# Kernel optimization log

Measured on AMD Instinct MI355X. Metric: run time of the kernel, lower is better.

The kernel has to match this reference:

```python
import jax, jax.numpy as jnp
import numpy as np

N = 100000      # nodes
E = 1600000     # edges (before self-loops)
IN_C = 128
HID = 256
L = 4
EPS = 1e-5


def setup_inputs() -> dict:
    key = jax.random.key(0)
    ks = jax.random.split(key, 12)
    s = 0.05
    x = jax.random.normal(ks[0], (N, IN_C), dtype=jnp.float32)
    edge_index = jax.random.randint(ks[1], (2, E), 0, N, dtype=jnp.int64)
    enc_w = jax.random.normal(ks[2], (IN_C, HID), dtype=jnp.float32) * s
    enc_b = jnp.zeros((HID,), jnp.float32)
    conv_w = jax.random.normal(ks[3], (L, HID, HID), dtype=jnp.float32) * s
    conv_b = jnp.zeros((L, HID), jnp.float32)
    ln_g = jnp.ones((L, HID), jnp.float32)
    ln_b = jnp.zeros((L, HID), jnp.float32)
    lin1_w = jax.random.normal(ks[4], (HID, HID // 2), dtype=jnp.float32) * s
    lin1_b = jnp.zeros((HID // 2,), jnp.float32)
    lin2_w = jax.random.normal(ks[5], (HID // 2, 1), dtype=jnp.float32) * s
    lin2_b = jnp.zeros((1,), jnp.float32)
    return dict(x=x, edge_index=edge_index, enc_w=enc_w, enc_b=enc_b,
                conv_w=conv_w, conv_b=conv_b, ln_g=ln_g, ln_b=ln_b,
                lin1_w=lin1_w, lin1_b=lin1_b, lin2_w=lin2_w, lin2_b=lin2_b)


def _layer_norm(h, g, b):
    mu = jnp.mean(h, axis=-1, keepdims=True)
    var = jnp.mean(jnp.square(h - mu), axis=-1, keepdims=True)
    return (h - mu) * jax.lax.rsqrt(var + EPS) * g + b


def reference(x, edge_index, enc_w, enc_b, conv_w, conv_b, ln_g, ln_b,
              lin1_w, lin1_b, lin2_w, lin2_b):
    loops = jnp.arange(N, dtype=edge_index.dtype)
    row = jnp.concatenate([edge_index[0], loops])   # source
    col = jnp.concatenate([edge_index[1], loops])   # target
    # GCN symmetric norm with self-loop weight 1 (improved=False)
    deg = jax.ops.segment_sum(jnp.ones(row.shape[0], jnp.float32), col,
                              num_segments=N)
    dis = jnp.where(deg > 0, jax.lax.rsqrt(deg), 0.0)  # deg^-1/2, [N]

    h = x @ enc_w + enc_b
    for i in range(L):
        hw = h @ conv_w[i]
        # norm_e = dis[row]*dis[col]: scale at source, aggregate, scale at target
        agg = jax.ops.segment_sum((hw * dis[:, None])[row], col,
                                  num_segments=N)
        h = agg * dis[:, None] + conv_b[i]
        h = jax.nn.relu(_layer_norm(h, ln_g[i], ln_b[i]))
        # dropout p=0.1 is identity in eval mode
    h = jax.nn.relu(h @ lin1_w + lin1_b)
    return h @ lin2_w + lin2_b  # [N, 1]
```

## Files before the change

kernel.cpp:

```cpp
#include <hip/hip_runtime.h>

#define N_NODES 100000
#define N_EDGES 1600000
#define IN_C    128
#define HID     256
#define NLAYER  4

#define NBUCK 391
#define BCAP  8192
#define EPB   4096
#define CAPL  6144

typedef __attribute__((ext_vector_type(8))) __bf16 bf16x8;
typedef __attribute__((ext_vector_type(4))) float  floatx4;

__device__ inline unsigned short f2b(float f) {
    unsigned u = __builtin_bit_cast(unsigned, f);
    return (unsigned short)((u + 0x7fffu + ((u >> 16) & 1u)) >> 16);
}
__device__ inline void acc8(float* a, uint4 v) {
    unsigned wds[4] = {v.x, v.y, v.z, v.w};
    #pragma unroll
    for (int k = 0; k < 4; ++k) {
        a[2*k]   += __builtin_bit_cast(float, wds[k] << 16);
        a[2*k+1] += __builtin_bit_cast(float, wds[k] & 0xffff0000u);
    }
}
__device__ inline void gl16(const void* g, void* l) {
    __builtin_amdgcn_global_load_lds(
        (const __attribute__((address_space(1))) unsigned int*)g,
        (__attribute__((address_space(3))) unsigned int*)l, 16, 0, 0);
}

__global__ __launch_bounds__(256) void kb_scatter(
        const int* __restrict__ row, const int* __restrict__ col,
        int* __restrict__ gfill, uint2* __restrict__ pairs, int e) {
    __shared__ uint2 ep[EPB];
    __shared__ int hist[NBUCK];
    __shared__ int lbase[NBUCK];
    const int tid  = threadIdx.x;
    const int base = blockIdx.x * EPB;
    for (int b = tid; b < NBUCK; b += 256) hist[b] = 0;
    __syncthreads();
    #pragma unroll
    for (int k = 0; k < EPB / 256; ++k) {
        int i = base + k * 256 + tid;
        uint2 pr = make_uint2(0xffffffffu, 0u);
        if (i < e) {
            pr.x = (unsigned)col[i];
            pr.y = (unsigned)row[i];
            atomicAdd(&hist[pr.x >> 8], 1);
        }
        ep[k * 256 + tid] = pr;
    }
    __syncthreads();
    for (int b = tid; b < NBUCK; b += 256) {
        int h = hist[b];
        lbase[b] = h ? atomicAdd(&gfill[b], h) : 0;
    }
    __syncthreads();
    for (int b = tid; b < NBUCK; b += 256) hist[b] = 0;
    __syncthreads();
    #pragma unroll
    for (int k = 0; k < EPB / 256; ++k) {
        uint2 pr = ep[k * 256 + tid];
        if (pr.x != 0xffffffffu) {
            int bk = pr.x >> 8;
            int p  = lbase[bk] + atomicAdd(&hist[bk], 1);
            if (p < BCAP) pairs[(size_t)bk * BCAP + p] = pr;
        }
    }
}

__global__ void kb_scan(const int* __restrict__ gfill, int* __restrict__ boff,
                        int* __restrict__ offs) {
    __shared__ int wsum[8];
    const int t = threadIdx.x, lane = t & 63, w = t >> 6;
    int v = (t < NBUCK) ? gfill[t] : 0;
    int inc = v;
    #pragma unroll
    for (int o = 1; o < 64; o <<= 1) { int u = __shfl_up(inc, o); if (lane >= o) inc += u; }
    if (lane == 63) wsum[w] = inc;
    __syncthreads();
    if (t == 0) { int r = 0; for (int i = 0; i < 8; ++i) { int x = wsum[i]; wsum[i] = r; r += x; } }
    __syncthreads();
    int excl = wsum[w] + inc - v;
    if (t <= NBUCK) boff[t] = excl;
    if (t == 0) offs[N_NODES] = N_EDGES;
}

__global__ __launch_bounds__(256) void kb_build(
        const uint2* __restrict__ pairs, const int* __restrict__ gfill,
        const int* __restrict__ boff,
        int* __restrict__ offs, float* __restrict__ dis,
        int* __restrict__ srcl, int n) {
    __shared__ int lcnt[256];
    __shared__ int lstart[256];
    __shared__ int wsum[4];
    __shared__ int sl[CAPL];
    const int b = blockIdx.x;
    const int tid = threadIdx.x, lane = tid & 63, w = tid >> 6;
    int cnt = gfill[b]; if (cnt > CAPL) cnt = CAPL;
    const int base = boff[b];
    const uint2* bp = pairs + (size_t)b * BCAP;
    lcnt[tid] = 0;
    __syncthreads();
    for (int i = tid; i < cnt; i += 256)
        atomicAdd(&lcnt[bp[i].x & 255], 1);
    __syncthreads();
    int v = lcnt[tid];
    int inc = v;
    #pragma unroll
    for (int o = 1; o < 64; o <<= 1) { int u = __shfl_up(inc, o); if (lane >= o) inc += u; }
    if (lane == 63) wsum[w] = inc;
    __syncthreads();
    if (tid == 0) { int r = 0; for (int i = 0; i < 4; ++i) { int x = wsum[i]; wsum[i] = r; r += x; } }
    __syncthreads();
    int excl = wsum[w] + inc - v;
    lstart[tid] = excl;
    int node = (b << 8) + tid;
    if (node < n) {
        dis[node]  = rsqrtf((float)(v + 1));
        offs[node] = base + excl;
    }
    __syncthreads();
    lcnt[tid] = 0;
    __syncthreads();
    for (int i = tid; i < cnt; i += 256) {
        uint2 pr = bp[i];
        int c = pr.x & 255;
        int q = lstart[c] + atomicAdd(&lcnt[c], 1);
        sl[q] = (int)pr.y;
    }
    __syncthreads();
    for (int i = tid; i < cnt; i += 256)
        srcl[base + i] = sl[i];
}

__global__ void k_wtz(const float* __restrict__ enc_w, const float* __restrict__ conv_w,
                      const float* __restrict__ w1,
                      unsigned short* __restrict__ enc_t, unsigned short* __restrict__ conv_t,
                      unsigned short* __restrict__ lin1_t, int* __restrict__ gfill) {
    int idx = blockIdx.x * blockDim.x + threadIdx.x;
    if (idx < NBUCK) gfill[idx] = 0;
    if (idx < IN_C * HID) {
        int k = idx / HID, n = idx % HID;
        enc_t[n * IN_C + k] = f2b(enc_w[idx]);
    } else if (idx < IN_C * HID + NLAYER * HID * HID) {
        int r = idx - IN_C * HID;
        int l = r / (HID * HID);
        int e = r % (HID * HID);
        int k = e / HID, n = e % HID;
        conv_t[(size_t)l * HID * HID + n * HID + k] = f2b(conv_w[r]);
    } else if (idx < IN_C * HID + NLAYER * HID * HID + HID * (HID / 2)) {
        int e = idx - (IN_C * HID + NLAYER * HID * HID);
        int k = e / (HID / 2), n = e % (HID / 2);
        lin1_t[n * HID + k] = f2b(w1[e]);
    }
}

__global__ __launch_bounds__(512) void k_mme(
        const float* __restrict__ Af,
        const unsigned short* __restrict__ Wt,
        const float* __restrict__ bias,
        unsigned short* __restrict__ Cout, int M) {
    const int K = IN_C;
    __shared__ unsigned short As[128 * 32];
    __shared__ unsigned short Bs[256 * 32];
    const int tid  = threadIdx.x;
    const int lane = tid & 63;
    const int w    = tid >> 6;
    const int bm   = blockIdx.x * 128;

    const int r0 = tid >> 2, q0 = tid & 3;
    const int a_off  = min(bm + r0, M - 1) * K + q0 * 8;
    const int b_off0 = r0 * K + q0 * 8;
    const int b_off1 = (r0 + 128) * K + q0 * 8;

    floatx4 acc[4][4];
    #pragma unroll
    for (int i = 0; i < 4; ++i)
        #pragma unroll
        for (int j = 0; j < 4; ++j)
            acc[i][j] = (floatx4){0.f, 0.f, 0.f, 0.f};

    const int wm = (w & 1) * 64;
    const int wn = (w >> 1) * 64;
    const int fm = lane & 15;
    const int fq = (lane >> 4) * 8;

    uint4 ra;
    auto loadA = [&](int koff, uint4& oa) {
        float4 f0 = *(const float4*)(Af + a_off + koff);
        float4 f1 = *(const float4*)(Af + a_off + koff + 4);
        oa.x = (unsigned)f2b(f0.x) | ((unsigned)f2b(f0.y) << 16);
        oa.y = (unsigned)f2b(f0.z) | ((unsigned)f2b(f0.w) << 16);
        oa.z = (unsigned)f2b(f1.x) | ((unsigned)f2b(f1.y) << 16);
        oa.w = (unsigned)f2b(f1.z) | ((unsigned)f2b(f1.w) << 16);
    };

    loadA(0, ra);

    const int KT = K >> 5;
    for (int kt = 0; kt < KT; ++kt) {
        int k0 = kt << 5;
        ((uint4*)As)[tid] = ra;
        gl16(Wt + b_off0 + k0, Bs + (size_t)tid * 8);
        gl16(Wt + b_off1 + k0, Bs + (size_t)(tid + 512) * 8);
        __syncthreads();
        if (kt + 1 < KT) loadA((kt + 1) << 5, ra);
        bf16x8 af[4], bfr[4];
        #pragma unroll
        for (int i = 0; i < 4; ++i)
            af[i] = *(const bf16x8*)(const void*)(As + (wm + i * 16 + fm) * 32 + fq);
        #pragma unroll
        for (int j = 0; j < 4; ++j)
            bfr[j] = *(const bf16x8*)(const void*)(Bs + (wn + j * 16 + fm) * 32 + fq);
        #pragma unroll
        for (int i = 0; i < 4; ++i)
            #pragma unroll
            for (int j = 0; j < 4; ++j)
                acc[i][j] = __builtin_amdgcn_mfma_f32_16x16x32_bf16(af[i], bfr[j], acc[i][j], 0, 0, 0);
        __syncthreads();
    }

    const int quad = lane >> 4;
    #pragma unroll
    for (int i = 0; i < 4; ++i) {
        #pragma unroll
        for (int r = 0; r < 4; ++r) {
            int row = bm + wm + i * 16 + quad * 4 + r;
            if (row >= M) continue;
            #pragma unroll
            for (int j = 0; j < 4; ++j) {
                int colg = wn + j * 16 + fm;
                float v = acc[i][j][r] + bias[colg];
                Cout[(size_t)row * HID + colg] = f2b(v);
            }
        }
    }
}

__global__ __launch_bounds__(512) void k_mmc(
        const unsigned short* __restrict__ A,
        const unsigned short* __restrict__ Wt,
        const float* __restrict__ scale,
        unsigned short* __restrict__ Cout, int M) {
    const int K = HID;
    __shared__ unsigned short As[128 * 32];
    __shared__ unsigned short Bs[256 * 32];
    const int tid  = threadIdx.x;
    const int lane = tid & 63;
    const int w    = tid >> 6;
    const int bm   = blockIdx.x * 128;

    const int r0 = tid >> 2, q0 = tid & 3;
    const int a_off  = min(bm + r0, M - 1) * K + q0 * 8;
    const int b_off0 = r0 * K + q0 * 8;
    const int b_off1 = (r0 + 128) * K + q0 * 8;

    floatx4 acc[4][4];
    #pragma unroll
    for (int i = 0; i < 4; ++i)
        #pragma unroll
        for (int j = 0; j < 4; ++j)
            acc[i][j] = (floatx4){0.f, 0.f, 0.f, 0.f};

    const int wm = (w & 1) * 64;
    const int wn = (w >> 1) * 64;
    const int fm = lane & 15;
    const int fq = (lane >> 4) * 8;

    for (int kt = 0; kt < 8; ++kt) {
        int k0 = kt << 5;
        gl16(A  + a_off  + k0, As + (size_t)tid * 8);
        gl16(Wt + b_off0 + k0, Bs + (size_t)tid * 8);
        gl16(Wt + b_off1 + k0, Bs + (size_t)(tid + 512) * 8);
        __syncthreads();
        bf16x8 af[4], bfr[4];
        #pragma unroll
        for (int i = 0; i < 4; ++i)
            af[i] = *(const bf16x8*)(const void*)(As + (wm + i * 16 + fm) * 32 + fq);
        #pragma unroll
        for (int j = 0; j < 4; ++j)
            bfr[j] = *(const bf16x8*)(const void*)(Bs + (wn + j * 16 + fm) * 32 + fq);
        #pragma unroll
        for (int i = 0; i < 4; ++i)
            #pragma unroll
            for (int j = 0; j < 4; ++j)
                acc[i][j] = __builtin_amdgcn_mfma_f32_16x16x32_bf16(af[i], bfr[j], acc[i][j], 0, 0, 0);
        __syncthreads();
    }

    const int quad = lane >> 4;
    #pragma unroll
    for (int i = 0; i < 4; ++i) {
        #pragma unroll
        for (int r = 0; r < 4; ++r) {
            int row = bm + wm + i * 16 + quad * 4 + r;
            if (row >= M) continue;
            float sc = scale[row];
            #pragma unroll
            for (int j = 0; j < 4; ++j) {
                int colg = wn + j * 16 + fm;
                Cout[(size_t)row * HID + colg] = f2b(acc[i][j][r] * sc);
            }
        }
    }
}

__global__ __launch_bounds__(256) void k_head(
        const unsigned short* __restrict__ A,
        const unsigned short* __restrict__ Wt,
        const float* __restrict__ b1, const float* __restrict__ w2,
        const float* __restrict__ b2, float* __restrict__ out, int M) {
    const int K = 256;
    __shared__ unsigned short As[128 * 32];
    __shared__ unsigned short Bs[128 * 32];
    const int tid  = threadIdx.x;
    const int lane = tid & 63;
    const int w    = tid >> 6;
    const int bm   = blockIdx.x * 128;

    const int i0 = tid, i1 = tid + 256;
    const int r0 = i0 >> 2, r1 = i1 >> 2;
    const int q0 = i0 & 3,  q1 = i1 & 3;
    const int a_off0 = min(bm + r0, M - 1) * K + q0 * 8;
    const int a_off1 = min(bm + r1, M - 1) * K + q1 * 8;
    const int b_off0 = r0 * K + q0 * 8;
    const int b_off1 = r1 * K + q1 * 8;

    floatx4 acc[4][4];
    #pragma unroll
    for (int i = 0; i < 4; ++i)
        #pragma unroll
        for (int j = 0; j < 4; ++j)
            acc[i][j] = (floatx4){0.f, 0.f, 0.f, 0.f};

    const int wm = (w & 1) * 64;
    const int wn = (w >> 1) * 64;
    const int fm = lane & 15;
    const int fq = (lane >> 4) * 8;

    for (int kt = 0; kt < 8; ++kt) {
        int k0 = kt << 5;
        gl16(A  + a_off0 + k0, As + (size_t)i0 * 8);
        gl16(A  + a_off1 + k0, As + (size_t)i1 * 8);
        gl16(Wt + b_off0 + k0, Bs + (size_t)i0 * 8);
        gl16(Wt + b_off1 + k0, Bs + (size_t)i1 * 8);
        __syncthreads();
        bf16x8 af[4], bfr[4];
        #pragma unroll
        for (int i = 0; i < 4; ++i)
            af[i] = *(const bf16x8*)(const void*)(As + (wm + i * 16 + fm) * 32 + fq);
        #pragma unroll
        for (int j = 0; j < 4; ++j)
            bfr[j] = *(const bf16x8*)(const void*)(Bs + (wn + j * 16 + fm) * 32 + fq);
        #pragma unroll
        for (int i = 0; i < 4; ++i)
            #pragma unroll
            for (int j = 0; j < 4; ++j)
                acc[i][j] = __builtin_amdgcn_mfma_f32_16x16x32_bf16(af[i], bfr[j], acc[i][j], 0, 0, 0);
        __syncthreads();
    }

    float* red = (float*)As;
    const int q = lane >> 4;
    float b1v[4], w2v[4];
    #pragma unroll
    for (int j = 0; j < 4; ++j) {
        int col = wn + j * 16 + fm;
        b1v[j] = b1[col]; w2v[j] = w2[col];
    }
    #pragma unroll
    for (int i = 0; i < 4; ++i) {
        #pragma unroll
        for (int r = 0; r < 4; ++r) {
            float s = 0.f;
            #pragma unroll
            for (int j = 0; j < 4; ++j)
                s += fmaxf(acc[i][j][r] + b1v[j], 0.f) * w2v[j];
            #pragma unroll
            for (int off = 1; off < 16; off <<= 1) s += __shfl_xor(s, off);
            if (fm == 0) {
                int m = wm + i * 16 + q * 4 + r;
                red[m * 2 + (wn >> 6)] = s;
            }
        }
    }
    __syncthreads();
    if (tid < 128) {
        int row = bm + tid;
        if (row < M) out[row] = red[tid * 2] + red[tid * 2 + 1] + b2[0];
    }
}

__global__ void k_agg(const unsigned short* __restrict__ hw, const int* __restrict__ srcl,
                      const int* __restrict__ offs, const float* __restrict__ dis,
                      const float* __restrict__ cb, const float* __restrict__ g,
                      const float* __restrict__ bt, unsigned short* __restrict__ hout, int n) {
    int gtid = blockIdx.x * blockDim.x + threadIdx.x;
    int node = __builtin_amdgcn_readfirstlane(gtid >> 6);
    int lane = threadIdx.x & 63;
    const int half = lane >> 5;
    const int sub  = lane & 31;
    const uint4* T = (const uint4*)hw;

    float a[8] = {0,0,0,0,0,0,0,0};
    float c[8] = {0,0,0,0,0,0,0,0};
    if (half == 0) {
        uint4 v = T[(size_t)node * 32 + sub];
        acc8(a, v);
    }
    int p = offs[node], pe = offs[node + 1];
    for (; p + 7 < pe; p += 8) {
        int s0 = srcl[p],     s1 = srcl[p + 1], s2 = srcl[p + 2], s3 = srcl[p + 3];
        int s4 = srcl[p + 4], s5 = srcl[p + 5], s6 = srcl[p + 6], s7 = srcl[p + 7];
        int ea = half ? s1 : s0;
        int eb = half ? s3 : s2;
        int ec = half ? s5 : s4;
        int ed = half ? s7 : s6;
        uint4 va = T[(size_t)ea * 32 + sub];
        uint4 vb = T[(size_t)eb * 32 + sub];
        uint4 vc = T[(size_t)ec * 32 + sub];
        uint4 vd = T[(size_t)ed * 32 + sub];
        acc8(a, va);
        acc8(c, vb);
        acc8(a, vc);
        acc8(c, vd);
    }
    for (; p + 1 < pe; p += 2) {
        int s0 = srcl[p], s1 = srcl[p + 1];
        int ea = half ? s1 : s0;
        uint4 v = T[(size_t)ea * 32 + sub];
        acc8(a, v);
    }
    if (p < pe && half == 0) {
        int s0 = srcl[p];
        uint4 v = T[(size_t)s0 * 32 + sub];
        acc8(a, v);
    }
    #pragma unroll
    for (int j = 0; j < 8; ++j) {
        a[j] += c[j];
        a[j] += __shfl_xor(a[j], 32);
    }
    float dc = dis[node];
    const float4* cb4 = (const float4*)cb;
    const float4* g4  = (const float4*)g;
    const float4* bt4 = (const float4*)bt;
    float4 cba = cb4[sub * 2], cbb = cb4[sub * 2 + 1];
    float h[8];
    h[0] = fmaf(a[0], dc, cba.x); h[1] = fmaf(a[1], dc, cba.y);
    h[2] = fmaf(a[2], dc, cba.z); h[3] = fmaf(a[3], dc, cba.w);
    h[4] = fmaf(a[4], dc, cbb.x); h[5] = fmaf(a[5], dc, cbb.y);
    h[6] = fmaf(a[6], dc, cbb.z); h[7] = fmaf(a[7], dc, cbb.w);
    float s = 0.f, sq = 0.f;
    #pragma unroll
    for (int j = 0; j < 8; ++j) { s += h[j]; sq += h[j] * h[j]; }
    #pragma unroll
    for (int off = 1; off < 32; off <<= 1) { s += __shfl_xor(s, off); sq += __shfl_xor(sq, off); }
    float mu  = s * (1.f / 256.f);
    float var = sq * (1.f / 256.f) - mu * mu;
    float inv = rsqrtf(var + 1e-5f);
    if (half == 0) {
        float4 ga = g4[sub * 2], gb = g4[sub * 2 + 1];
        float4 ba = bt4[sub * 2], bb = bt4[sub * 2 + 1];
        float gv[8] = {ga.x, ga.y, ga.z, ga.w, gb.x, gb.y, gb.z, gb.w};
        float bv[8] = {ba.x, ba.y, ba.z, ba.w, bb.x, bb.y, bb.z, bb.w};
        unsigned short o[8];
        #pragma unroll
        for (int j = 0; j < 8; ++j)
            o[j] = f2b(fmaxf(fmaf((h[j] - mu) * inv, gv[j], bv[j]), 0.f));
        uint4 st;
        st.x = (unsigned)o[0] | ((unsigned)o[1] << 16);
        st.y = (unsigned)o[2] | ((unsigned)o[3] << 16);
        st.z = (unsigned)o[4] | ((unsigned)o[5] << 16);
        st.w = (unsigned)o[6] | ((unsigned)o[7] << 16);
        ((uint4*)hout)[(size_t)node * 32 + sub] = st;
    }
}

extern "C" void kernel_launch(void* const* d_in, const int* in_sizes, int n_in,
                              void* d_out, int out_size, void* d_ws, size_t ws_size,
                              hipStream_t stream) {
    const float* x      = (const float*)d_in[0];
    const int*   ei     = (const int*)d_in[1];
    const float* enc_w  = (const float*)d_in[2];
    const float* enc_b  = (const float*)d_in[3];
    const float* conv_w = (const float*)d_in[4];
    const float* conv_b = (const float*)d_in[5];
    const float* ln_g   = (const float*)d_in[6];
    const float* ln_b   = (const float*)d_in[7];
    const float* w1     = (const float*)d_in[8];
    const float* b1     = (const float*)d_in[9];
    const float* w2     = (const float*)d_in[10];
    const float* b2     = (const float*)d_in[11];
    float* out = (float*)d_out;

    char* ws = (char*)d_ws;
    size_t off = 0;
    auto alloc = [&](size_t bytes) -> void* {
        void* p = ws + off;
        off = (off + bytes + 255) & ~(size_t)255;
        return p;
    };
    int*   offs  = (int*)alloc((size_t)(N_NODES + 1) * 4);
    int*   srcl  = (int*)alloc((size_t)N_EDGES * 4);
    float* dis   = (float*)alloc((size_t)N_NODES * 4);
    int*   gfill = (int*)alloc((size_t)NBUCK * 4);
    int*   boff  = (int*)alloc((size_t)(NBUCK + 1) * 4);
    unsigned short* hb = (unsigned short*)alloc((size_t)N_NODES * HID * 2);
    unsigned short* hw = (unsigned short*)alloc((size_t)N_NODES * HID * 2);
    uint2* pairs = (uint2*)alloc((size_t)NBUCK * BCAP * 8);
    unsigned short* enc_t  = (unsigned short*)alloc((size_t)IN_C * HID * 2);
    unsigned short* conv_t = (unsigned short*)alloc((size_t)NLAYER * HID * HID * 2);
    unsigned short* lin1_t = (unsigned short*)alloc((size_t)HID * (HID / 2) * 2);

    const int* row = ei;
    const int* col = ei + N_EDGES;

    {
        int tot = IN_C * HID + NLAYER * HID * HID + HID * (HID / 2);
        k_wtz<<<(tot + 255) / 256, 256, 0, stream>>>(enc_w, conv_w, w1,
                                                     enc_t, conv_t, lin1_t, gfill);
    }
    kb_scatter<<<(N_EDGES + EPB - 1) / EPB, 256, 0, stream>>>(row, col, gfill, pairs, N_EDGES);
    kb_scan<<<1, 512, 0, stream>>>(gfill, boff, offs);
    kb_build<<<NBUCK, 256, 0, stream>>>(pairs, gfill, boff, offs, dis, srcl, N_NODES);

    k_mme<<<(N_NODES + 127) / 128, 512, 0, stream>>>(x, enc_t, enc_b, hb, N_NODES);

    for (int l = 0; l < NLAYER; ++l) {
        k_mmc<<<(N_NODES + 127) / 128, 512, 0, stream>>>(
            hb, conv_t + (size_t)l * HID * HID, dis, hw, N_NODES);
        k_agg<<<(N_NODES * 64 + 255) / 256, 256, 0, stream>>>(
            hw, srcl, offs, dis, conv_b + l * HID, ln_g + l * HID, ln_b + l * HID, hb, N_NODES);
    }

    k_head<<<(N_NODES + 127) / 128, 256, 0, stream>>>(hb, lin1_t, b1, w2, b2, out, N_NODES);
}
```

Baseline: 779.8 us.

## Pack edge pairs, locally sort scatter, drop scan kernel, pipeline aggregation loads

The CSR build now packs each (row, col-low-byte) pair into one 32-bit word and sorts edges by bucket in shared memory, so the global writes to the bucket arrays are contiguous. The separate single-block scan kernel is gone: each build block computes its own bucket base by summing gfill, and offs[N] is set in the weight-transpose kernel. The aggregation kernel software-pipelines the neighbour gathers, issuing the next batch of loads before accumulating the current one, and accumulates with packed v_pk_add_f32. This trades extra register pressure and redundant prefix sums for less launch overhead, less memory traffic and better latency hiding. Packing the row index into 24 bits works because N is 100000.

```diff
diff --git a/kernel.cpp b/kernel.cpp
--- a/kernel.cpp
+++ b/kernel.cpp
@@ -13,17 +13,25 @@
 
 typedef __attribute__((ext_vector_type(8))) __bf16 bf16x8;
 typedef __attribute__((ext_vector_type(4))) float  floatx4;
+typedef __attribute__((ext_vector_type(2))) float  floatx2;
 
 __device__ inline unsigned short f2b(float f) {
     unsigned u = __builtin_bit_cast(unsigned, f);
     return (unsigned short)((u + 0x7fffu + ((u >> 16) & 1u)) >> 16);
 }
-__device__ inline void acc8(float* a, uint4 v) {
+__device__ inline floatx2 pkadd(floatx2 x, floatx2 y) {
+    floatx2 r;
+    asm("v_pk_add_f32 %0, %1, %2" : "=v"(r) : "v"(x), "v"(y));
+    return r;
+}
+__device__ inline void acc8p(floatx2* a, uint4 v) {
     unsigned wds[4] = {v.x, v.y, v.z, v.w};
     #pragma unroll
     for (int k = 0; k < 4; ++k) {
-        a[2*k]   += __builtin_bit_cast(float, wds[k] << 16);
-        a[2*k+1] += __builtin_bit_cast(float, wds[k] & 0xffff0000u);
+        floatx2 x;
+        x[0] = __builtin_bit_cast(float, wds[k] << 16);
+        x[1] = __builtin_bit_cast(float, wds[k] & 0xffff0000u);
+        a[k] = pkadd(a[k], x);
     }
 }
 __device__ inline void gl16(const void* g, void* l) {
@@ -34,80 +42,99 @@
 
 __global__ __launch_bounds__(256) void kb_scatter(
         const int* __restrict__ row, const int* __restrict__ col,
-        int* __restrict__ gfill, uint2* __restrict__ pairs, int e) {
-    __shared__ uint2 ep[EPB];
+        int* __restrict__ gfill, unsigned* __restrict__ pairs, int e) {
+    __shared__ unsigned sp[EPB];
+    __shared__ unsigned short sbk[EPB];
     __shared__ int hist[NBUCK];
+    __shared__ int lpre[NBUCK];
     __shared__ int lbase[NBUCK];
-    const int tid  = threadIdx.x;
+    __shared__ int wsum[4];
+    __shared__ int carry;
+    const int tid = threadIdx.x, lane = tid & 63, w = tid >> 6;
     const int base = blockIdx.x * EPB;
+    const int nv   = min(EPB, e - base);
     for (int b = tid; b < NBUCK; b += 256) hist[b] = 0;
     __syncthreads();
     #pragma unroll
     for (int k = 0; k < EPB / 256; ++k) {
         int i = base + k * 256 + tid;
-        uint2 pr = make_uint2(0xffffffffu, 0u);
-        if (i < e) {
-            pr.x = (unsigned)col[i];
-            pr.y = (unsigned)row[i];
-            atomicAdd(&hist[pr.x >> 8], 1);
-        }
-        ep[k * 256 + tid] = pr;
+        if (i < e) atomicAdd(&hist[((unsigned)col[i]) >> 8], 1);
     }
     __syncthreads();
     for (int b = tid; b < NBUCK; b += 256) {
         int h = hist[b];
         lbase[b] = h ? atomicAdd(&gfill[b], h) : 0;
     }
+    {
+        int v = hist[tid];
+        int inc = v;
+        #pragma unroll
+        for (int o = 1; o < 64; o <<= 1) { int u = __shfl_up(inc, o); if (lane >= o) inc += u; }
+        if (lane == 63) wsum[w] = inc;
+        __syncthreads();
+        if (tid == 0) { int r = 0; for (int i = 0; i < 4; ++i) { int x = wsum[i]; wsum[i] = r; r += x; } carry = r; }
+        __syncthreads();
+        lpre[tid] = wsum[w] + inc - v;
+        int c0 = carry;
+        __syncthreads();
+        int idx = 256 + tid;
+        int v1 = (idx < NBUCK) ? hist[idx] : 0;
+        int inc1 = v1;
+        #pragma unroll
+        for (int o = 1; o < 64; o <<= 1) { int u = __shfl_up(inc1, o); if (lane >= o) inc1 += u; }
+        if (lane == 63) wsum[w] = inc1;
+        __syncthreads();
+        if (tid == 0) { int r = 0; for (int i = 0; i < 4; ++i) { int x = wsum[i]; wsum[i] = r; r += x; } }
+        __syncthreads();
+        if (idx < NBUCK) lpre[idx] = c0 + wsum[w] + inc1 - v1;
+    }
     __syncthreads();
     for (int b = tid; b < NBUCK; b += 256) hist[b] = 0;
     __syncthreads();
     #pragma unroll
     for (int k = 0; k < EPB / 256; ++k) {
-        uint2 pr = ep[k * 256 + tid];
-        if (pr.x != 0xffffffffu) {
-            int bk = pr.x >> 8;
-            int p  = lbase[bk] + atomicAdd(&hist[bk], 1);
-            if (p < BCAP) pairs[(size_t)bk * BCAP + p] = pr;
+        int i = base + k * 256 + tid;
+        if (i < e) {
+            unsigned cv = (unsigned)col[i];
+            int bk = cv >> 8;
+            int q = lpre[bk] + atomicAdd(&hist[bk], 1);
+            sp[q]  = ((unsigned)row[i] << 8) | (cv & 255u);
+            sbk[q] = (unsigned short)bk;
         }
     }
-}
-
-__global__ void kb_scan(const int* __restrict__ gfill, int* __restrict__ boff,
-                        int* __restrict__ offs) {
-    __shared__ int wsum[8];
-    const int t = threadIdx.x, lane = t & 63, w = t >> 6;
-    int v = (t < NBUCK) ? gfill[t] : 0;
-    int inc = v;
-    #pragma unroll
-    for (int o = 1; o < 64; o <<= 1) { int u = __shfl_up(inc, o); if (lane >= o) inc += u; }
-    if (lane == 63) wsum[w] = inc;
-    __syncthreads();
-    if (t == 0) { int r = 0; for (int i = 0; i < 8; ++i) { int x = wsum[i]; wsum[i] = r; r += x; } }
-    __syncthreads();
-    int excl = wsum[w] + inc - v;
-    if (t <= NBUCK) boff[t] = excl;
-    if (t == 0) offs[N_NODES] = N_EDGES;
+    __syncthreads();
+    for (int i = tid; i < nv; i += 256) {
+        int bk = sbk[i];
+        int pos = lbase[bk] + (i - lpre[bk]);
+        if (pos < BCAP) pairs[(size_t)bk * BCAP + pos] = sp[i];
+    }
 }
 
 __global__ __launch_bounds__(256) void kb_build(
-        const uint2* __restrict__ pairs, const int* __restrict__ gfill,
-        const int* __restrict__ boff,
+        const unsigned* __restrict__ pairs, const int* __restrict__ gfill,
         int* __restrict__ offs, float* __restrict__ dis,
         int* __restrict__ srcl, int n) {
     __shared__ int lcnt[256];
     __shared__ int lstart[256];
     __shared__ int wsum[4];
+    __shared__ int sbase;
     __shared__ int sl[CAPL];
     const int b = blockIdx.x;
     const int tid = threadIdx.x, lane = tid & 63, w = tid >> 6;
     int cnt = gfill[b]; if (cnt > CAPL) cnt = CAPL;
-    const int base = boff[b];
-    const uint2* bp = pairs + (size_t)b * BCAP;
+    const unsigned* bp = pairs + (size_t)b * BCAP;
+    int pa = 0;
+    for (int i = tid; i < b; i += 256) pa += gfill[i];
+    #pragma unroll
+    for (int o = 1; o < 64; o <<= 1) pa += __shfl_xor(pa, o);
     lcnt[tid] = 0;
-    __syncthreads();
+    if (lane == 0) wsum[w] = pa;
+    __syncthreads();
+    if (tid == 0) sbase = wsum[0] + wsum[1] + wsum[2] + wsum[3];
     for (int i = tid; i < cnt; i += 256)
-        atomicAdd(&lcnt[bp[i].x & 255], 1);
-    __syncthreads();
+        atomicAdd(&lcnt[bp[i] & 255u], 1);
+    __syncthreads();
+    const int base = sbase;
     int v = lcnt[tid];
     int inc = v;
     #pragma unroll
@@ -127,10 +154,10 @@
     lcnt[tid] = 0;
     __syncthreads();
     for (int i = tid; i < cnt; i += 256) {
-        uint2 pr = bp[i];
-        int c = pr.x & 255;
+        unsigned pr = bp[i];
+        int c = pr & 255u;
         int q = lstart[c] + atomicAdd(&lcnt[c], 1);
-        sl[q] = (int)pr.y;
+        sl[q] = (int)(pr >> 8);
     }
     __syncthreads();
     for (int i = tid; i < cnt; i += 256)
@@ -140,8 +167,10 @@
 __global__ void k_wtz(const float* __restrict__ enc_w, const float* __restrict__ conv_w,
                       const float* __restrict__ w1,
                       unsigned short* __restrict__ enc_t, unsigned short* __restrict__ conv_t,
-                      unsigned short* __restrict__ lin1_t, int* __restrict__ gfill) {
+                      unsigned short* __restrict__ lin1_t, int* __restrict__ gfill,
+                      int* __restrict__ offs) {
     int idx = blockIdx.x * blockDim.x + threadIdx.x;
+    if (idx == 0) offs[N_NODES] = N_EDGES;
     if (idx < NBUCK) gfill[idx] = 0;
     if (idx < IN_C * HID) {
         int k = idx / HID, n = idx % HID;
@@ -406,44 +435,51 @@
     const int sub  = lane & 31;
     const uint4* T = (const uint4*)hw;
 
-    float a[8] = {0,0,0,0,0,0,0,0};
-    float c[8] = {0,0,0,0,0,0,0,0};
-    if (half == 0) {
-        uint4 v = T[(size_t)node * 32 + sub];
-        acc8(a, v);
-    }
+    floatx2 a2[4], c2[4];
+    #pragma unroll
+    for (int k = 0; k < 4; ++k) { a2[k] = (floatx2)0.f; c2[k] = (floatx2)0.f; }
+    if (half == 0)
+        acc8p(a2, T[(size_t)node * 32 + sub]);
+
     int p = offs[node], pe = offs[node + 1];
-    for (; p + 7 < pe; p += 8) {
-        int s0 = srcl[p],     s1 = srcl[p + 1], s2 = srcl[p + 2], s3 = srcl[p + 3];
-        int s4 = srcl[p + 4], s5 = srcl[p + 5], s6 = srcl[p + 6], s7 = srcl[p + 7];
-        int ea = half ? s1 : s0;
-        int eb = half ? s3 : s2;
-        int ec = half ? s5 : s4;
-        int ed = half ? s7 : s6;
-        uint4 va = T[(size_t)ea * 32 + sub];
-        uint4 vb = T[(size_t)eb * 32 + sub];
-        uint4 vc = T[(size_t)ec * 32 + sub];
-        uint4 vd = T[(size_t)ed * 32 + sub];
-        acc8(a, va);
-        acc8(c, vb);
-        acc8(a, vc);
-        acc8(c, vd);
+    if (p + 7 < pe) {
+        uint4 va, vb, vc, vd;
+        {
+            int s0 = srcl[p],     s1 = srcl[p + 1], s2 = srcl[p + 2], s3 = srcl[p + 3];
+            int s4 = srcl[p + 4], s5 = srcl[p + 5], s6 = srcl[p + 6], s7 = srcl[p + 7];
+            int ea = half ? s1 : s0, eb = half ? s3 : s2;
+            int ec = half ? s5 : s4, ed = half ? s7 : s6;
+            va = T[(size_t)ea * 32 + sub]; vb = T[(size_t)eb * 32 + sub];
+            vc = T[(size_t)ec * 32 + sub]; vd = T[(size_t)ed * 32 + sub];
+        }
+        for (p += 8; p + 7 < pe; p += 8) {
+            int s0 = srcl[p],     s1 = srcl[p + 1], s2 = srcl[p + 2], s3 = srcl[p + 3];
+            int s4 = srcl[p + 4], s5 = srcl[p + 5], s6 = srcl[p + 6], s7 = srcl[p + 7];
+            int ea = half ? s1 : s0, eb = half ? s3 : s2;
+            int ec = half ? s5 : s4, ed = half ? s7 : s6;
+            uint4 wa = T[(size_t)ea * 32 + sub];
+            uint4 wb = T[(size_t)eb * 32 + sub];
+            uint4 wc = T[(size_t)ec * 32 + sub];
+            uint4 wd = T[(size_t)ed * 32 + sub];
+            acc8p(a2, va); acc8p(c2, vb); acc8p(a2, vc); acc8p(c2, vd);
+            va = wa; vb = wb; vc = wc; vd = wd;
+        }
+        acc8p(a2, va); acc8p(c2, vb); acc8p(a2, vc); acc8p(c2, vd);
     }
     for (; p + 1 < pe; p += 2) {
         int s0 = srcl[p], s1 = srcl[p + 1];
         int ea = half ? s1 : s0;
-        uint4 v = T[(size_t)ea * 32 + sub];
-        acc8(a, v);
-    }
-    if (p < pe && half == 0) {
-        int s0 = srcl[p];
-        uint4 v = T[(size_t)s0 * 32 + sub];
-        acc8(a, v);
-    }
-    #pragma unroll
-    for (int j = 0; j < 8; ++j) {
-        a[j] += c[j];
-        a[j] += __shfl_xor(a[j], 32);
+        acc8p(a2, T[(size_t)ea * 32 + sub]);
+    }
+    if (p < pe && half == 0)
+        acc8p(a2, T[(size_t)srcl[p] * 32 + sub]);
+
+    float af[8];
+    #pragma unroll
+    for (int k = 0; k < 4; ++k) {
+        floatx2 t = pkadd(a2[k], c2[k]);
+        af[2 * k]     = t[0] + __shfl_xor(t[0], 32);
+        af[2 * k + 1] = t[1] + __shfl_xor(t[1], 32);
     }
     float dc = dis[node];
     const float4* cb4 = (const float4*)cb;
@@ -451,10 +487,10 @@
     const float4* bt4 = (const float4*)bt;
     float4 cba = cb4[sub * 2], cbb = cb4[sub * 2 + 1];
     float h[8];
-    h[0] = fmaf(a[0], dc, cba.x); h[1] = fmaf(a[1], dc, cba.y);
-    h[2] = fmaf(a[2], dc, cba.z); h[3] = fmaf(a[3], dc, cba.w);
-    h[4] = fmaf(a[4], dc, cbb.x); h[5] = fmaf(a[5], dc, cbb.y);
-    h[6] = fmaf(a[6], dc, cbb.z); h[7] = fmaf(a[7], dc, cbb.w);
+    h[0] = fmaf(af[0], dc, cba.x); h[1] = fmaf(af[1], dc, cba.y);
+    h[2] = fmaf(af[2], dc, cba.z); h[3] = fmaf(af[3], dc, cba.w);
+    h[4] = fmaf(af[4], dc, cbb.x); h[5] = fmaf(af[5], dc, cbb.y);
+    h[6] = fmaf(af[6], dc, cbb.z); h[7] = fmaf(af[7], dc, cbb.w);
     float s = 0.f, sq = 0.f;
     #pragma unroll
     for (int j = 0; j < 8; ++j) { s += h[j]; sq += h[j] * h[j]; }
@@ -509,10 +545,9 @@
     int*   srcl  = (int*)alloc((size_t)N_EDGES * 4);
     float* dis   = (float*)alloc((size_t)N_NODES * 4);
     int*   gfill = (int*)alloc((size_t)NBUCK * 4);
-    int*   boff  = (int*)alloc((size_t)(NBUCK + 1) * 4);
     unsigned short* hb = (unsigned short*)alloc((size_t)N_NODES * HID * 2);
     unsigned short* hw = (unsigned short*)alloc((size_t)N_NODES * HID * 2);
-    uint2* pairs = (uint2*)alloc((size_t)NBUCK * BCAP * 8);
+    unsigned* pairs = (unsigned*)alloc((size_t)NBUCK * BCAP * 4);
     unsigned short* enc_t  = (unsigned short*)alloc((size_t)IN_C * HID * 2);
     unsigned short* conv_t = (unsigned short*)alloc((size_t)NLAYER * HID * HID * 2);
     unsigned short* lin1_t = (unsigned short*)alloc((size_t)HID * (HID / 2) * 2);
@@ -523,11 +558,10 @@
     {
         int tot = IN_C * HID + NLAYER * HID * HID + HID * (HID / 2);
         k_wtz<<<(tot + 255) / 256, 256, 0, stream>>>(enc_w, conv_w, w1,
-                                                     enc_t, conv_t, lin1_t, gfill);
+                                                     enc_t, conv_t, lin1_t, gfill, offs);
     }
     kb_scatter<<<(N_EDGES + EPB - 1) / EPB, 256, 0, stream>>>(row, col, gfill, pairs, N_EDGES);
-    kb_scan<<<1, 512, 0, stream>>>(gfill, boff, offs);
-    kb_build<<<NBUCK, 256, 0, stream>>>(pairs, gfill, boff, offs, dis, srcl, N_NODES);
+    kb_build<<<NBUCK, 256, 0, stream>>>(pairs, gfill, offs, dis, srcl, N_NODES);
 
     k_mme<<<(N_NODES + 127) / 128, 512, 0, stream>>>(x, enc_t, enc_b, hb, N_NODES);
 
```

After: 787.2 us. No clear change (+1.0%).
